# Optimization experiments

Hardware: AMD Instinct MI355X
Metric: run time of the kernel (lower is better)

The kernel has to match this reference:

```python
import jax, jax.numpy as jnp
import numpy as np

B, C, O, K, H, W, R = 32, 256, 256, 3, 56, 56, 16  # batch, in, out, kernel, spatial, reduction

def setup_inputs() -> dict:
    key = jax.random.key(0)
    ks = jax.random.split(key, 10)
    x = jax.random.normal(ks[0], (B, C, H, W), jnp.float32)
    # kaiming_normal fan_out: std = sqrt(2 / (O * K * K))
    base_w = jax.random.normal(ks[1], (O, C, K, K), jnp.float32) * np.sqrt(2.0 / (O * K * K))
    def lin(kw, kb, out_f, in_f):
        bound = 1.0 / np.sqrt(in_f)
        w = jax.random.uniform(kw, (out_f, in_f), jnp.float32, -bound, bound)
        b = jax.random.uniform(kb, (out_f,), jnp.float32, -bound, bound)
        return w, b
    fc_share_w, fc_share_b = lin(ks[2], ks[3], R, C)
    fc_inp_w, fc_inp_b = lin(ks[4], ks[5], C, R)   # in_planes // groups = C
    fc_oup_w, fc_oup_b = lin(ks[6], ks[7], O, R)
    fc_k_w, fc_k_b = lin(ks[8], ks[9], K * K, R)
    return {"x": x, "base_w": base_w,
            "fc_share_w": fc_share_w, "fc_share_b": fc_share_b,
            "fc_inp_w": fc_inp_w, "fc_inp_b": fc_inp_b,
            "fc_oup_w": fc_oup_w, "fc_oup_b": fc_oup_b,
            "fc_k_w": fc_k_w, "fc_k_b": fc_k_b}

def reference(x, base_w, fc_share_w, fc_share_b, fc_inp_w, fc_inp_b,
              fc_oup_w, fc_oup_b, fc_k_w, fc_k_b):
    # Attn4d: global avg pool -> shared FC -> three sigmoid branches
    s = jnp.mean(x, axis=(2, 3))                                   # [B, C]
    h = jax.nn.relu(s @ fc_share_w.T + fc_share_b)                 # [B, R]
    a_inp = jax.nn.sigmoid(h @ fc_inp_w.T + fc_inp_b)              # [B, C]
    a_oup = jax.nn.sigmoid(h @ fc_oup_w.T + fc_oup_b)              # [B, O]
    a_k = jax.nn.sigmoid(h @ fc_k_w.T + fc_k_b)                    # [B, K*K]
    # rank-1 outer products -> per-sample 4D attention [B, O, C, K, K]
    attn = jnp.einsum('bo,bi,bk->boik', a_oup, a_inp, a_k)
    attn = attn.reshape(x.shape[0], base_w.shape[0], base_w.shape[1],
                        base_w.shape[2], base_w.shape[3])
    w = base_w[None] * attn                                        # [B, O, C, K, K]
    # per-sample conv (equivalent to the groups=B grouped-conv trick)
    def conv1(xi, wi):
        return jax.lax.conv_general_dilated(
            xi[None], wi, window_strides=(1, 1),
            padding=((1, 1), (1, 1)),
            dimension_numbers=('NCHW', 'OIHW', 'NCHW'))[0]
    return jax.vmap(conv1)(x, w)                                   # [B, O, H, W]
```

## Files before the change

kernel.cpp:

```cpp
#include <hip/hip_runtime.h>


typedef __attribute__((ext_vector_type(8))) short s16x8;
typedef __attribute__((ext_vector_type(4))) float fx4;

#define PP_FIRST 59
#define XTP_ROWS 3456

__device__ __forceinline__ unsigned short bf16_rne(float f){
  unsigned u = __builtin_bit_cast(unsigned, f);
  u += 0x7fffu + ((u >> 16) & 1u);
  return (unsigned short)(u >> 16);
}
__device__ __forceinline__ float bf16_to_f(unsigned short h){
  unsigned u = ((unsigned)h) << 16;
  return __builtin_bit_cast(float, u);
}

__global__ void zpad_kernel(unsigned short* __restrict__ xtp, float* __restrict__ s){
  const int slot = blockIdx.x, r = blockIdx.y;
  const int t = threadIdx.x;
  if(r == 0) s[(slot << 8) + t] = 0.f;
  const int row = (r < 59) ? r : (3305 + (r - 59));
  xtp[((size_t)slot * XTP_ROWS + row) * 256 + t] = 0;
}

__global__ void xpool_kernel(const float* __restrict__ x,
                             unsigned short* __restrict__ xtp,
                             float* __restrict__ s){
  const int c0 = blockIdx.x * 64, h = blockIdx.y;
  const int b = blockIdx.z;
  __shared__ float tile[64 * 59];
  const int t = threadIdx.x;
  const float* xb = x + ((size_t)b * 256 + c0) * 3136 + h * 56;
  for(int i = t; i < 1792; i += 256){
    int c = i / 28, w2 = (i % 28) * 2;
    float2 v = *(const float2*)(xb + (size_t)c * 3136 + w2);
    tile[c * 59 + w2]     = v.x;
    tile[c * 59 + w2 + 1] = v.y;
  }
  __syncthreads();
  {
    const int c = t >> 2, q = t & 3;
    float sm = 0.f;
    for(int w = q; w < 56; w += 4) sm += tile[c * 59 + w];
    sm += __shfl_down(sm, 2, 4);
    sm += __shfl_down(sm, 1, 4);
    if(q == 0) atomicAdd(&s[(b << 8) + c0 + c], sm);
  }
  const size_t base = ((size_t)b * XTP_ROWS + (size_t)(h + 1) * 58) * 256 + c0;
  for(int i = t; i < 58 * 32; i += 256){
    int wp = i >> 5, cp = (i & 31) * 2;
    float v0 = 0.f, v1 = 0.f;
    if(wp >= 1 && wp <= 56){
      v0 = tile[cp * 59 + (wp - 1)];
      v1 = tile[(cp + 1) * 59 + (wp - 1)];
    }
    unsigned short h0 = bf16_rne(v0), h1 = bf16_rne(v1);
    *(unsigned*)(xtp + base + (size_t)wp * 256 + cp) = (unsigned)h0 | ((unsigned)h1 << 16);
  }
}

__global__ void fc_kernel(const float* __restrict__ s,
                          const float* __restrict__ shw, const float* __restrict__ shb,
                          const float* __restrict__ inw, const float* __restrict__ inb,
                          const float* __restrict__ ouw, const float* __restrict__ oub,
                          const float* __restrict__ kw,  const float* __restrict__ kb,
                          float* __restrict__ a_inp, float* __restrict__ aoup_s,
                          float* __restrict__ rho, int* __restrict__ tpk){
  __shared__ float hh[32*16];
  __shared__ float ak[32*9];
  __shared__ float akmax[32];
  const int t = threadIdx.x;
  for(int i = t; i < 512; i += 256){
    int b = i >> 4, r = i & 15;
    float dot = 0.f;
    const float* sp = s + b*256; const float* wp = shw + r*256;
    for(int c = 0; c < 256; ++c) dot += sp[c] * wp[c];
    hh[i] = fmaxf(shb[r] + dot * (1.0f / 3136.0f), 0.f);
  }
  __syncthreads();
  for(int i = t; i < 288; i += 256){
    int b = i / 9, k = i % 9;
    float acc = kb[k];
    for(int r = 0; r < 16; ++r) acc += hh[b*16+r] * kw[k*16+r];
    ak[i] = 1.f / (1.f + expf(-acc));
  }
  __syncthreads();
  if(t < 32){
    float v[9]; int id[9];
    for(int j = 0; j < 9; ++j){ v[j] = ak[t*9 + j]; id[j] = j; }
    for(int a = 1; a < 9; ++a){
      float vv = v[a]; int ii = id[a]; int p = a - 1;
      while(p >= 0 && v[p] > vv){ v[p+1] = v[p]; id[p+1] = id[p]; --p; }
      v[p+1] = vv; id[p+1] = ii;
    }
    for(int j = 0; j < 9; ++j){
      tpk[t*32 + 2*j]     = id[j];
      tpk[t*32 + 2*j + 1] = (id[j]/3 - 1)*58 + (id[j]%3 - 1);
    }
    for(int j = 0; j < 8; ++j) rho[t*8 + j] = v[j] / v[j+1];
    akmax[t] = v[8];
  }
  __syncthreads();
  for(int i = t; i < 8192; i += 256){
    int b = i >> 8, c = i & 255;
    float acc = inb[c];
    for(int r = 0; r < 16; ++r) acc += hh[b*16+r] * inw[c*16+r];
    a_inp[i] = 1.f / (1.f + expf(-acc));
  }
  for(int i = t; i < 8192; i += 256){
    int b = i >> 8, o = i & 255;
    float acc = oub[o];
    for(int r = 0; r < 16; ++r) acc += hh[b*16+r] * ouw[o*16+r];
    aoup_s[i] = (1.f / (1.f + expf(-acc))) * akmax[b];
  }
}

__global__ void wsplit_kernel(const float* __restrict__ bw, const float* __restrict__ a_inp,
                              unsigned short* __restrict__ wt_hi,
                              unsigned short* __restrict__ wt_lo, int b0){
  const int o = blockIdx.x, slot = blockIdx.y;
  const int c = threadIdx.x;
  const int b = b0 + slot;
  const float ai = a_inp[(b << 8) + c];
  const float* p = bw + ((size_t)o * 256 + c) * 9;
  #pragma unroll
  for(int k = 0; k < 9; ++k){
    float v = p[k] * ai;
    unsigned short h = bf16_rne(v);
    unsigned short l = bf16_rne(v - bf16_to_f(h));
    size_t idx = (((size_t)slot * 9 + k) * 256 + o) * 256 + c;
    wt_hi[idx] = h; wt_lo[idx] = l;
  }
}

#define GLDS(gp, lo_) __builtin_amdgcn_global_load_lds( \
    (const __attribute__((address_space(1))) void*)(gp), \
    (__attribute__((address_space(3))) void*)(lds + (lo_)), 16, 0, 0)

__launch_bounds__(256, 2)
__global__ void conv_kernel(const unsigned short* __restrict__ wt_hi,
                            const unsigned short* __restrict__ wt_lo,
                            const unsigned short* __restrict__ xtp,
                            const float* __restrict__ aoup_s,
                            const float* __restrict__ rho,
                            const int* __restrict__ tpk,
                            float* __restrict__ out, int b0){
  __shared__ unsigned char lds[65536];
  const int tile = blockIdx.x;
  const int o0   = blockIdx.y << 7;
  const int slot = blockIdx.z;
  const int b    = b0 + slot;
  const int pp0  = PP_FIRST + tile * 256;
  const int t    = threadIdx.x;
  const int lane = t & 63;
  const int wave = t >> 6;
  const int wm = wave >> 1, wn = wave & 1;

  fx4 acc[4][8];
  #pragma unroll
  for(int i = 0; i < 4; ++i)
    #pragma unroll
    for(int j = 0; j < 8; ++j)
      acc[i][j] = fx4{0.f, 0.f, 0.f, 0.f};

  const int srow = t >> 3;
  const int sg8  = (((t & 7) ^ ((t >> 3) & 7)) << 3);
  const int ldsu = wave << 10;

  const int rA  = lane & 15;
  const int kg  = lane >> 4;
  const int r7  = rA & 7;
  const int gk0 = ((kg ^ r7) << 4);
  const int gk1 = (((4 + kg) ^ r7) << 4);
  const int aRow = ((wm << 6) + rA) * 128;
  const int bRow = ((wn << 7) + rA) * 128;

  const size_t xrow0 = (size_t)b * XTP_ROWS * 256;
  const size_t wrow0 = (size_t)slot * 9 * 65536;

  for(int tap = 0; tap < 9; ++tap){
    if(tap > 0){
      const float rr = rho[(b << 3) + tap - 1];
      #pragma unroll
      for(int i = 0; i < 4; ++i)
        #pragma unroll
        for(int j = 0; j < 8; ++j)
          #pragma unroll
          for(int r = 0; r < 4; ++r) acc[i][j][r] *= rr;
    }
    const int pt  = tpk[(b << 5) + (tap << 1)];
    const int off = tpk[(b << 5) + (tap << 1) + 1];
    const unsigned short* xp  = xtp + xrow0 + (size_t)(pp0 + off + srow) * 256 + sg8;
    const unsigned short* wh0 = wt_hi + wrow0 + ((size_t)(pt * 256 + o0 + srow)) * 256 + sg8;
    const unsigned short* wl0 = wt_lo + wrow0 + ((size_t)(pt * 256 + o0 + srow)) * 256 + sg8;

    for(int cc = 0; cc < 4; ++cc){
      const int co = cc << 6;
      #pragma unroll
      for(int rnd = 0; rnd < 8; ++rnd)
        GLDS(xp + co + rnd * 8192, 0 + rnd * 4096 + ldsu);
      #pragma unroll
      for(int rnd = 0; rnd < 4; ++rnd){
        GLDS(wh0 + co + rnd * 8192, 32768 + rnd * 4096 + ldsu);
        GLDS(wl0 + co + rnd * 8192, 49152 + rnd * 4096 + ldsu);
      }
      __syncthreads();
      #pragma unroll
      for(int ks = 0; ks < 2; ++ks){
        const int gk = ks ? gk1 : gk0;
        s16x8 ah[4], al[4], bh[8];
        #pragma unroll
        for(int i = 0; i < 4; ++i){
          const int ro = aRow + i * 2048 + gk;
          ah[i] = *(const s16x8*)(lds + 32768 + ro);
          al[i] = *(const s16x8*)(lds + 49152 + ro);
        }
        #pragma unroll
        for(int j = 0; j < 8; ++j)
          bh[j] = *(const s16x8*)(lds + bRow + j * 2048 + gk);
        #pragma unroll
        for(int i = 0; i < 4; ++i)
          #pragma unroll
          for(int j = 0; j < 8; ++j){
            acc[i][j] = __builtin_amdgcn_mfma_f32_16x16x32_bf16(ah[i], bh[j], acc[i][j], 0, 0, 0);
            acc[i][j] = __builtin_amdgcn_mfma_f32_16x16x32_bf16(al[i], bh[j], acc[i][j], 0, 0, 0);
          }
      }
      __syncthreads();
    }
  }

  float sc[4][4];
  #pragma unroll
  for(int i = 0; i < 4; ++i){
    const int ob = o0 + (wm << 6) + i * 16 + (kg << 2);
    #pragma unroll
    for(int r = 0; r < 4; ++r) sc[i][r] = aoup_s[(b << 8) + ob + r];
  }
  #pragma unroll
  for(int j = 0; j < 8; ++j){
    const int pp = pp0 + (wn << 7) + j * 16 + rA;
    const int hp = pp / 58, wp = pp % 58;
    if(hp >= 1 && hp <= 56 && wp >= 1 && wp <= 56){
      const int p = (hp - 1) * 56 + (wp - 1);
      #pragma unroll
      for(int i = 0; i < 4; ++i){
        const int ob = o0 + (wm << 6) + i * 16 + (kg << 2);
        float* op = out + ((size_t)((b << 8) + ob)) * 3136 + p;
        #pragma unroll
        for(int r = 0; r < 4; ++r) op[(size_t)r * 3136] = acc[i][j][r] * sc[i][r];
      }
    }
  }
}

extern "C" void kernel_launch(void* const* d_in, const int* in_sizes, int n_in,
                              void* d_out, int out_size, void* d_ws, size_t ws_size,
                              hipStream_t stream){
  const float* x   = (const float*)d_in[0];
  const float* bw  = (const float*)d_in[1];
  const float* shw = (const float*)d_in[2];
  const float* shb = (const float*)d_in[3];
  const float* inw = (const float*)d_in[4];
  const float* inb = (const float*)d_in[5];
  const float* ouw = (const float*)d_in[6];
  const float* oub = (const float*)d_in[7];
  const float* kw  = (const float*)d_in[8];
  const float* kb  = (const float*)d_in[9];
  float* out = (float*)d_out;

  char* ws = (char*)d_ws;
  float* s      = (float*)(ws);
  float* a_inp  = (float*)(ws + 32768);
  float* aoup_s = (float*)(ws + 65536);
  float* rho    = (float*)(ws + 98304);
  int*   tpk    = (int*)(ws + 99328);
  unsigned short* xtp   = (unsigned short*)(ws + 103424);
  unsigned short* wt_hi = (unsigned short*)(ws + 56726528);

  const size_t WBYTES = 2359296;
  size_t chw = (ws_size > 56726528) ? (ws_size - 56726528) / WBYTES : 1;
  if(chw > 32) chw = 32; if(chw < 1) chw = 1;
  const int CH_W = (int)chw;
  unsigned short* wt_lo = wt_hi + (size_t)CH_W * 9 * 65536;

  hipLaunchKernelGGL(zpad_kernel,  dim3(32, 210), dim3(256), 0, stream, xtp, s);
  hipLaunchKernelGGL(xpool_kernel, dim3(4, 56, 32), dim3(256), 0, stream, x, xtp, s);
  hipLaunchKernelGGL(fc_kernel,    dim3(1), dim3(256), 0, stream,
                     s, shw, shb, inw, inb, ouw, oub, kw, kb, a_inp, aoup_s, rho, tpk);
  for(int b0 = 0; b0 < 32; b0 += CH_W){
    const int z = (32 - b0 < CH_W) ? (32 - b0) : CH_W;
    hipLaunchKernelGGL(wsplit_kernel, dim3(256, z), dim3(256), 0, stream,
                       bw, a_inp, wt_hi, wt_lo, b0);
    hipLaunchKernelGGL(conv_kernel,   dim3(13, 2, z), dim3(256), 0, stream,
                       wt_hi, wt_lo, xtp, aoup_s, rho, tpk, out, b0);
  }
}
```

Baseline: 516.4 us.

## Fold input-channel attention into activations and share one weight split across batch

```diff
diff --git a/kernel.cpp b/kernel.cpp
--- a/kernel.cpp
+++ b/kernel.cpp
@@ -27,6 +27,7 @@
 
 __global__ void xpool_kernel(const float* __restrict__ x,
                              unsigned short* __restrict__ xtp,
+                             unsigned short* __restrict__ xlo,
                              float* __restrict__ s){
   const int c0 = blockIdx.x * 64, h = blockIdx.y;
   const int b = blockIdx.z;
@@ -58,6 +59,12 @@
     }
     unsigned short h0 = bf16_rne(v0), h1 = bf16_rne(v1);
     *(unsigned*)(xtp + base + (size_t)wp * 256 + cp) = (unsigned)h0 | ((unsigned)h1 << 16);
+    if(wp >= 1 && wp <= 56){
+      unsigned short l0 = bf16_rne(v0 - bf16_to_f(h0));
+      unsigned short l1 = bf16_rne(v1 - bf16_to_f(h1));
+      size_t li = (((size_t)b * 3136) + h * 56 + (wp - 1)) * 256 + c0 + cp;
+      *(unsigned*)(xlo + li) = (unsigned)l0 | ((unsigned)l1 << 16);
+    }
   }
 }
 
@@ -117,20 +124,38 @@
   }
 }
 
-__global__ void wsplit_kernel(const float* __restrict__ bw, const float* __restrict__ a_inp,
+__global__ void xscale_kernel(unsigned short* __restrict__ xtp,
+                              const unsigned short* __restrict__ xlo,
+                              const float* __restrict__ a_inp){
+  const int h = blockIdx.x, b = blockIdx.y;
+  const int t = threadIdx.x;
+  __shared__ float as[256];
+  as[t] = a_inp[(b << 8) + t];
+  __syncthreads();
+  for(int p = t; p < 7168; p += 256){
+    const int w = p >> 7, cp2 = p & 127;
+    const int g = (h + 1) * 58 + (w + 1);
+    unsigned* hp = (unsigned*)(xtp + ((size_t)b * XTP_ROWS + g) * 256 + cp2 * 2);
+    const unsigned lo = *(const unsigned*)(xlo + (((size_t)b * 3136) + h * 56 + w) * 256 + cp2 * 2);
+    const unsigned hi = *hp;
+    const float v0 = (bf16_to_f((unsigned short)hi) + bf16_to_f((unsigned short)lo)) * as[cp2*2];
+    const float v1 = (bf16_to_f((unsigned short)(hi >> 16)) + bf16_to_f((unsigned short)(lo >> 16))) * as[cp2*2+1];
+    *hp = (unsigned)bf16_rne(v0) | ((unsigned)bf16_rne(v1) << 16);
+  }
+}
+
+__global__ void wsplit_kernel(const float* __restrict__ bw,
                               unsigned short* __restrict__ wt_hi,
-                              unsigned short* __restrict__ wt_lo, int b0){
-  const int o = blockIdx.x, slot = blockIdx.y;
-  const int c = threadIdx.x;
-  const int b = b0 + slot;
-  const float ai = a_inp[(b << 8) + c];
-  const float* p = bw + ((size_t)o * 256 + c) * 9;
+                              unsigned short* __restrict__ wt_lo){
+  const int i = blockIdx.x * 256 + threadIdx.x;
+  const float* p = bw + (size_t)i * 9;
+  const int o = i >> 8, c = i & 255;
   #pragma unroll
   for(int k = 0; k < 9; ++k){
-    float v = p[k] * ai;
+    float v = p[k];
     unsigned short h = bf16_rne(v);
     unsigned short l = bf16_rne(v - bf16_to_f(h));
-    size_t idx = (((size_t)slot * 9 + k) * 256 + o) * 256 + c;
+    size_t idx = ((size_t)k << 16) + ((size_t)o << 8) + c;
     wt_hi[idx] = h; wt_lo[idx] = l;
   }
 }
@@ -146,12 +171,11 @@
                             const float* __restrict__ aoup_s,
                             const float* __restrict__ rho,
                             const int* __restrict__ tpk,
-                            float* __restrict__ out, int b0){
+                            float* __restrict__ out){
   __shared__ unsigned char lds[65536];
   const int tile = blockIdx.x;
   const int o0   = blockIdx.y << 7;
-  const int slot = blockIdx.z;
-  const int b    = b0 + slot;
+  const int b    = blockIdx.z;
   const int pp0  = PP_FIRST + tile * 256;
   const int t    = threadIdx.x;
   const int lane = t & 63;
@@ -178,7 +202,6 @@
   const int bRow = ((wn << 7) + rA) * 128;
 
   const size_t xrow0 = (size_t)b * XTP_ROWS * 256;
-  const size_t wrow0 = (size_t)slot * 9 * 65536;
 
   for(int tap = 0; tap < 9; ++tap){
     if(tap > 0){
@@ -193,8 +216,8 @@
     const int pt  = tpk[(b << 5) + (tap << 1)];
     const int off = tpk[(b << 5) + (tap << 1) + 1];
     const unsigned short* xp  = xtp + xrow0 + (size_t)(pp0 + off + srow) * 256 + sg8;
-    const unsigned short* wh0 = wt_hi + wrow0 + ((size_t)(pt * 256 + o0 + srow)) * 256 + sg8;
-    const unsigned short* wl0 = wt_lo + wrow0 + ((size_t)(pt * 256 + o0 + srow)) * 256 + sg8;
+    const unsigned short* wh0 = wt_hi + ((size_t)(pt * 256 + o0 + srow)) * 256 + sg8;
+    const unsigned short* wl0 = wt_lo + ((size_t)(pt * 256 + o0 + srow)) * 256 + sg8;
 
     for(int cc = 0; cc < 4; ++cc){
       const int co = cc << 6;
@@ -278,23 +301,16 @@
   float* rho    = (float*)(ws + 98304);
   int*   tpk    = (int*)(ws + 99328);
   unsigned short* xtp   = (unsigned short*)(ws + 103424);
-  unsigned short* wt_hi = (unsigned short*)(ws + 56726528);
-
-  const size_t WBYTES = 2359296;
-  size_t chw = (ws_size > 56726528) ? (ws_size - 56726528) / WBYTES : 1;
-  if(chw > 32) chw = 32; if(chw < 1) chw = 1;
-  const int CH_W = (int)chw;
-  unsigned short* wt_lo = wt_hi + (size_t)CH_W * 9 * 65536;
-
-  hipLaunchKernelGGL(zpad_kernel,  dim3(32, 210), dim3(256), 0, stream, xtp, s);
-  hipLaunchKernelGGL(xpool_kernel, dim3(4, 56, 32), dim3(256), 0, stream, x, xtp, s);
-  hipLaunchKernelGGL(fc_kernel,    dim3(1), dim3(256), 0, stream,
+  unsigned short* xlo   = (unsigned short*)(ws + 56726528);
+  unsigned short* wt_hi = (unsigned short*)(ws + 108106752);
+  unsigned short* wt_lo = (unsigned short*)(ws + 109286400);
+
+  hipLaunchKernelGGL(zpad_kernel,   dim3(32, 210),   dim3(256), 0, stream, xtp, s);
+  hipLaunchKernelGGL(xpool_kernel,  dim3(4, 56, 32), dim3(256), 0, stream, x, xtp, xlo, s);
+  hipLaunchKernelGGL(wsplit_kernel, dim3(256),       dim3(256), 0, stream, bw, wt_hi, wt_lo);
+  hipLaunchKernelGGL(fc_kernel,     dim3(1),         dim3(256), 0, stream,
                      s, shw, shb, inw, inb, ouw, oub, kw, kb, a_inp, aoup_s, rho, tpk);
-  for(int b0 = 0; b0 < 32; b0 += CH_W){
-    const int z = (32 - b0 < CH_W) ? (32 - b0) : CH_W;
-    hipLaunchKernelGGL(wsplit_kernel, dim3(256, z), dim3(256), 0, stream,
-                       bw, a_inp, wt_hi, wt_lo, b0);
-    hipLaunchKernelGGL(conv_kernel,   dim3(13, 2, z), dim3(256), 0, stream,
-                       wt_hi, wt_lo, xtp, aoup_s, rho, tpk, out, b0);
-  }
-}
+  hipLaunchKernelGGL(xscale_kernel, dim3(56, 32),    dim3(256), 0, stream, xtp, xlo, a_inp);
+  hipLaunchKernelGGL(conv_kernel,   dim3(13, 2, 32), dim3(256), 0, stream,
+                     wt_hi, wt_lo, xtp, aoup_s, rho, tpk, out);
+}
```

Measured after the change: 508.9 us. No clear change (-1.5%).
